# Performance work log

Measured on AMD Instinct MI355X. Metric: run time of the kernel, lower is better.

The kernel has to match this reference:

```python
import jax, jax.numpy as jnp
import numpy as np

N_NODES = 262144      # 2048 graphs * 128 nodes each
NUM_GRAPHS = 2048
MAX_NODES = 128
HIDDEN = 256
OUT_CH = 12
N_EDGES = 2097152     # ~avg degree 8


def setup_inputs() -> dict:
    key = jax.random.key(0)
    k1, k2, k3, k4 = jax.random.split(key, 4)
    x = jax.random.normal(k1, (N_NODES, HIDDEN), dtype=jnp.float32)
    # xavier-ish projection weight for Linear(6*hidden -> 12)
    W = jax.random.normal(k2, (OUT_CH, 6 * HIDDEN), dtype=jnp.float32) * (1.0 / np.sqrt(6 * HIDDEN))
    b = jnp.zeros((OUT_CH,), dtype=jnp.float32)
    # uniform graphs: sorted batch ids, MAX_NODES nodes per graph
    batch = (jnp.arange(N_NODES, dtype=jnp.int32) // MAX_NODES).astype(jnp.int32)
    # edges sampled within graphs: pick graph, then two local node ids
    g = jax.random.randint(k3, (N_EDGES,), 0, NUM_GRAPHS, dtype=jnp.int32)
    loc = jax.random.randint(k4, (N_EDGES, 2), 0, MAX_NODES, dtype=jnp.int32)
    src = g * MAX_NODES + loc[:, 0]
    dst = g * MAX_NODES + loc[:, 1]
    edge_index = jnp.stack([src, dst], axis=0).astype(jnp.int32)
    return {"x": x, "W": W, "b": b, "batch": batch, "edge_index": edge_index,
            "num_graphs": NUM_GRAPHS, "max_nodes": MAX_NODES}


def reference(x, W, b, batch, edge_index, num_graphs, max_nodes):
    N, H = x.shape
    G, M = num_graphs, max_nodes
    # local index of each node within its graph (batch is sorted by graph)
    counts = jax.ops.segment_sum(jnp.ones((N,), dtype=jnp.int32), batch, num_segments=G)
    starts = jnp.cumsum(counts) - counts            # exclusive prefix sum => first node of each graph
    local = jnp.arange(N, dtype=jnp.int32) - starts[batch]
    # dense per-graph node features X [G, M, H]
    X = jnp.zeros((G, M, H), dtype=x.dtype).at[batch, local].set(x)
    # dense symmetric adjacency A [G, M, M] (assignment semantics, like the torch loop)
    gi = batch[edge_index[0]]
    li = local[edge_index[0]]
    lj = local[edge_index[1]]
    A = jnp.zeros((G, M, M), dtype=x.dtype)
    A = A.at[gi, li, lj].set(1.0)
    A = A.at[gi, lj, li].set(1.0)
    # 6-gram walk readouts
    walk = X
    vs = [walk.sum(axis=1)]                          # v1
    for _ in range(5):                               # v2..v6
        walk = jnp.einsum('gnm,gmh->gnh', A, walk) * X
        vs.append(walk.sum(axis=1))
    out = jnp.concatenate(vs, axis=-1)               # == stack(dim=1).reshape(G, 6*H)
    out = out @ W.T + b                              # n_gram_projection
    return out
```

## Files before the change

### kernel.cpp

```cpp
#include <hip/hip_runtime.h>
#include <stdint.h>

#define NGRAPH 2048
#define MNODES 128
#define HID 256
#define OUTC 12
#define NEDGE 2097152

typedef __attribute__((ext_vector_type(8))) short short8;
typedef __attribute__((ext_vector_type(4))) float v4f;

#define SLICE 64
#define SWT_STRIDE 136

__device__ __forceinline__ unsigned short f2bf(float f) {
    unsigned int u = __builtin_bit_cast(unsigned int, f);
    u += 0x7fffu + ((u >> 16) & 1u);
    return (unsigned short)(u >> 16);
}

__global__ void build_bytes(const int* __restrict__ ei, unsigned char* __restrict__ Ab) {
    int e = blockIdx.x * blockDim.x + threadIdx.x;
    if (e >= NEDGE) return;
    int sN = ei[e];
    int dN = ei[NEDGE + e];
    int g = sN >> 7;
    int li = sN & 127;
    int lj = dN & 127;
    unsigned char* base = Ab + (size_t)g * (MNODES * MNODES);
    base[li * 128 + lj] = 1;
    base[lj * 128 + li] = 1;
}

__global__ void build_bits(const int* __restrict__ ei, unsigned int* __restrict__ bits) {
    int e = blockIdx.x * blockDim.x + threadIdx.x;
    if (e >= NEDGE) return;
    int sN = ei[e];
    int dN = ei[NEDGE + e];
    int g = sN >> 7;
    int li = sN & 127;
    int lj = dN & 127;
    unsigned int* base = bits + (size_t)g * (MNODES * 4);
    atomicOr(&base[li * 4 + (lj >> 5)], 1u << (lj & 31));
    atomicOr(&base[lj * 4 + (li >> 5)], 1u << (li & 31));
}

__launch_bounds__(256, 3)
__global__ void walk2(const float* __restrict__ x,
                      const float* __restrict__ W,
                      const unsigned char* __restrict__ Abytes,
                      const unsigned int* __restrict__ Abits,
                      int use_bytes,
                      float* __restrict__ partial) {
    __shared__ unsigned short sWT[SLICE][SWT_STRIDE];
    __shared__ float sVs2[2][6][SLICE];

    const int bx = blockIdx.x;
    const int g = bx >> 2;
    const int s = bx & 3;
    const int tid = threadIdx.x;
    const int wave = tid >> 6;
    const int lane = tid & 63;
    const int lrow = lane & 15;
    const int quad = lane >> 4;
    const int rhalf = wave >> 1;
    const int r0 = rhalf * 64;
    const int c0 = (wave & 1) * 32;
    const int cg0 = s * SLICE + c0;

    short8 areg[4][4];
    if (use_bytes) {
        const unsigned char* Ag = Abytes + (size_t)g * (MNODES * MNODES);
#pragma unroll
        for (int rt = 0; rt < 4; rt++) {
            int row = r0 + rt * 16 + lrow;
#pragma unroll
            for (int ks = 0; ks < 4; ks++) {
                int k0 = ks * 32 + quad * 8;
                uint2 u = *(const uint2*)(Ag + row * 128 + k0);
                short8 a;
#pragma unroll
                for (int j = 0; j < 8; j++) {
                    unsigned int byte = ((j < 4 ? u.x >> (8 * j) : u.y >> (8 * (j - 4))) & 0xFFu);
                    a[j] = (short)(byte ? 0x3F80 : 0);
                }
                areg[rt][ks] = a;
            }
        }
    } else {
        const unsigned int* Bg = Abits + (size_t)g * (MNODES * 4);
#pragma unroll
        for (int rt = 0; rt < 4; rt++) {
            int row = r0 + rt * 16 + lrow;
#pragma unroll
            for (int ks = 0; ks < 4; ks++) {
                unsigned int w = Bg[row * 4 + ks] >> (quad * 8);
                short8 a;
#pragma unroll
                for (int j = 0; j < 8; j++)
                    a[j] = (short)(((w >> j) & 1u) ? 0x3F80 : 0);
                areg[rt][ks] = a;
            }
        }
    }

    float xf[4][2][4];
    const float* xg = x + (size_t)g * (MNODES * HID);
#pragma unroll
    for (int rt = 0; rt < 4; rt++)
#pragma unroll
        for (int ct = 0; ct < 2; ct++) {
            int col = cg0 + ct * 16 + lrow;
#pragma unroll
            for (int reg = 0; reg < 4; reg++) {
                int row = r0 + rt * 16 + quad * 4 + reg;
                xf[rt][ct][reg] = xg[row * HID + col];
            }
        }
#pragma unroll
    for (int ct = 0; ct < 2; ct++) {
        int lcol = c0 + ct * 16 + lrow;
        float cs = 0.0f;
#pragma unroll
        for (int rt = 0; rt < 4; rt++) {
            int nbase = r0 + rt * 16 + quad * 4;
            uint2 u;
            u.x = (unsigned)f2bf(xf[rt][ct][0]) | ((unsigned)f2bf(xf[rt][ct][1]) << 16);
            u.y = (unsigned)f2bf(xf[rt][ct][2]) | ((unsigned)f2bf(xf[rt][ct][3]) << 16);
            *(uint2*)&sWT[lcol][nbase] = u;
            cs += xf[rt][ct][0] + xf[rt][ct][1] + xf[rt][ct][2] + xf[rt][ct][3];
        }
        cs += __shfl_xor(cs, 16);
        cs += __shfl_xor(cs, 32);
        if (quad == 0) sVs2[rhalf][0][lcol] = cs;
    }
    __syncthreads();

    for (int it = 1; it <= 5; it++) {
        v4f acc[4][2];
#pragma unroll
        for (int rt = 0; rt < 4; rt++)
#pragma unroll
            for (int ct = 0; ct < 2; ct++) acc[rt][ct] = (v4f)(0.0f);
#pragma unroll
        for (int ks = 0; ks < 4; ks++) {
            int k0 = ks * 32 + quad * 8;
#pragma unroll
            for (int ct = 0; ct < 2; ct++) {
                short8 bf = *(const short8*)&sWT[c0 + ct * 16 + lrow][k0];
#pragma unroll
                for (int rt = 0; rt < 4; rt++)
                    acc[rt][ct] = __builtin_amdgcn_mfma_f32_16x16x32_bf16(areg[rt][ks], bf, acc[rt][ct], 0, 0, 0);
            }
        }
        __syncthreads();
#pragma unroll
        for (int ct = 0; ct < 2; ct++) {
            int lcol = c0 + ct * 16 + lrow;
            float cs = 0.0f;
#pragma unroll
            for (int rt = 0; rt < 4; rt++) {
                float nw0 = acc[rt][ct][0] * xf[rt][ct][0];
                float nw1 = acc[rt][ct][1] * xf[rt][ct][1];
                float nw2 = acc[rt][ct][2] * xf[rt][ct][2];
                float nw3 = acc[rt][ct][3] * xf[rt][ct][3];
                int nbase = r0 + rt * 16 + quad * 4;
                uint2 u;
                u.x = (unsigned)f2bf(nw0) | ((unsigned)f2bf(nw1) << 16);
                u.y = (unsigned)f2bf(nw2) | ((unsigned)f2bf(nw3) << 16);
                *(uint2*)&sWT[lcol][nbase] = u;
                cs += nw0 + nw1 + nw2 + nw3;
            }
            cs += __shfl_xor(cs, 16);
            cs += __shfl_xor(cs, 32);
            if (quad == 0) sVs2[rhalf][it][lcol] = cs;
        }
        __syncthreads();
    }

    if (wave == 0) {
        for (int c = 0; c < OUTC; c++) {
            float p = 0.0f;
            const float* wr = W + c * (6 * HID);
#pragma unroll
            for (int ii = 0; ii < 6; ii++) {
                int i = ii * 64 + lane;
                int k = i >> 6;
                int h = i & 63;
                float v = sVs2[0][k][h] + sVs2[1][k][h];
                p += v * wr[k * HID + s * SLICE + h];
            }
#pragma unroll
            for (int off = 32; off >= 1; off >>= 1) p += __shfl_down(p, off);
            if (lane == 0) partial[bx * OUTC + c] = p;
        }
    }
}

__global__ void combine(const float* __restrict__ partial, const float* __restrict__ bvec,
                        float* __restrict__ out) {
    int i = blockIdx.x * blockDim.x + threadIdx.x;
    if (i >= NGRAPH * OUTC) return;
    int c = i % OUTC;
    int g = i / OUTC;
    float p = bvec[c];
#pragma unroll
    for (int s = 0; s < 4; s++) p += partial[(g * 4 + s) * OUTC + c];
    out[i] = p;
}

extern "C" void kernel_launch(void* const* d_in, const int* in_sizes, int n_in,
                              void* d_out, int out_size, void* d_ws, size_t ws_size,
                              hipStream_t stream) {
    const float* x = (const float*)d_in[0];
    const float* W = (const float*)d_in[1];
    const float* b = (const float*)d_in[2];
    const int* ei = (const int*)d_in[4];
    float* out = (float*)d_out;

    const size_t ABYTES = (size_t)NGRAPH * MNODES * MNODES;
    const size_t PARTIAL = (size_t)NGRAPH * 4 * OUTC * sizeof(float);

    if (ws_size >= ABYTES + PARTIAL) {
        unsigned char* Ab = (unsigned char*)d_ws;
        float* partial = (float*)((char*)d_ws + ABYTES);
        hipMemsetAsync(Ab, 0, ABYTES, stream);
        build_bytes<<<NEDGE / 256, 256, 0, stream>>>(ei, Ab);
        walk2<<<NGRAPH * 4, 256, 0, stream>>>(x, W, Ab, nullptr, 1, partial);
        combine<<<(NGRAPH * OUTC + 255) / 256, 256, 0, stream>>>(partial, b, out);
    } else {
        unsigned int* bits = (unsigned int*)d_ws;
        float* partial = (float*)((char*)d_ws + (size_t)NGRAPH * MNODES * 4 * 4);
        hipMemsetAsync(bits, 0, (size_t)NGRAPH * MNODES * 4 * 4, stream);
        build_bits<<<NEDGE / 512, 512, 0, stream>>>(ei, bits);
        walk2<<<NGRAPH * 4, 256, 0, stream>>>(x, W, nullptr, bits, 0, partial);
        combine<<<(NGRAPH * OUTC + 255) / 256, 256, 0, stream>>>(partial, b, out);
    }
}
```

Baseline: 502.6 us.

## Always use bitmask adjacency, hardware bf16 packing, and spread projection across waves

Drops the byte-per-entry adjacency path, which needs a 32MB memset and scatter plus 32MB of reads, and always builds a packed bitmask (4MB) with atomicOr. Each row's bitmask is now read as a single uint4. The manual round-to-nearest bf16 conversion is replaced with the v_cvt_pk_bf16_f32 instruction. The final projection is split across all four waves (three outputs each) instead of only wave 0, and launch bounds are raised to 5 blocks per SM, which risks register spills. Atomics in the bit build may contend within each graph's 2KB region.

```diff
diff --git a/kernel.cpp b/kernel.cpp
--- a/kernel.cpp
+++ b/kernel.cpp
@@ -13,23 +13,10 @@
 #define SLICE 64
 #define SWT_STRIDE 136
 
-__device__ __forceinline__ unsigned short f2bf(float f) {
-    unsigned int u = __builtin_bit_cast(unsigned int, f);
-    u += 0x7fffu + ((u >> 16) & 1u);
-    return (unsigned short)(u >> 16);
-}
-
-__global__ void build_bytes(const int* __restrict__ ei, unsigned char* __restrict__ Ab) {
-    int e = blockIdx.x * blockDim.x + threadIdx.x;
-    if (e >= NEDGE) return;
-    int sN = ei[e];
-    int dN = ei[NEDGE + e];
-    int g = sN >> 7;
-    int li = sN & 127;
-    int lj = dN & 127;
-    unsigned char* base = Ab + (size_t)g * (MNODES * MNODES);
-    base[li * 128 + lj] = 1;
-    base[lj * 128 + li] = 1;
+__device__ __forceinline__ unsigned int cvtpk_bf16(float lo, float hi) {
+    unsigned int r;
+    asm("v_cvt_pk_bf16_f32 %0, %1, %2" : "=v"(r) : "v"(lo), "v"(hi));
+    return r;
 }
 
 __global__ void build_bits(const int* __restrict__ ei, unsigned int* __restrict__ bits) {
@@ -45,12 +32,10 @@
     atomicOr(&base[lj * 4 + (li >> 5)], 1u << (li & 31));
 }
 
-__launch_bounds__(256, 3)
+__launch_bounds__(256, 5)
 __global__ void walk2(const float* __restrict__ x,
                       const float* __restrict__ W,
-                      const unsigned char* __restrict__ Abytes,
                       const unsigned int* __restrict__ Abits,
-                      int use_bytes,
                       float* __restrict__ partial) {
     __shared__ unsigned short sWT[SLICE][SWT_STRIDE];
     __shared__ float sVs2[2][6][SLICE];
@@ -69,32 +54,14 @@
     const int cg0 = s * SLICE + c0;
 
     short8 areg[4][4];
-    if (use_bytes) {
-        const unsigned char* Ag = Abytes + (size_t)g * (MNODES * MNODES);
+    {
+        const uint4* Bg = (const uint4*)(Abits + (size_t)g * (MNODES * 4));
 #pragma unroll
         for (int rt = 0; rt < 4; rt++) {
-            int row = r0 + rt * 16 + lrow;
+            uint4 w4 = Bg[r0 + rt * 16 + lrow];
 #pragma unroll
             for (int ks = 0; ks < 4; ks++) {
-                int k0 = ks * 32 + quad * 8;
-                uint2 u = *(const uint2*)(Ag + row * 128 + k0);
-                short8 a;
-#pragma unroll
-                for (int j = 0; j < 8; j++) {
-                    unsigned int byte = ((j < 4 ? u.x >> (8 * j) : u.y >> (8 * (j - 4))) & 0xFFu);
-                    a[j] = (short)(byte ? 0x3F80 : 0);
-                }
-                areg[rt][ks] = a;
-            }
-        }
-    } else {
-        const unsigned int* Bg = Abits + (size_t)g * (MNODES * 4);
-#pragma unroll
-        for (int rt = 0; rt < 4; rt++) {
-            int row = r0 + rt * 16 + lrow;
-#pragma unroll
-            for (int ks = 0; ks < 4; ks++) {
-                unsigned int w = Bg[row * 4 + ks] >> (quad * 8);
+                unsigned int w = (ks == 0 ? w4.x : ks == 1 ? w4.y : ks == 2 ? w4.z : w4.w) >> (quad * 8);
                 short8 a;
 #pragma unroll
                 for (int j = 0; j < 8; j++)
@@ -125,8 +92,8 @@
         for (int rt = 0; rt < 4; rt++) {
             int nbase = r0 + rt * 16 + quad * 4;
             uint2 u;
-            u.x = (unsigned)f2bf(xf[rt][ct][0]) | ((unsigned)f2bf(xf[rt][ct][1]) << 16);
-            u.y = (unsigned)f2bf(xf[rt][ct][2]) | ((unsigned)f2bf(xf[rt][ct][3]) << 16);
+            u.x = cvtpk_bf16(xf[rt][ct][0], xf[rt][ct][1]);
+            u.y = cvtpk_bf16(xf[rt][ct][2], xf[rt][ct][3]);
             *(uint2*)&sWT[lcol][nbase] = u;
             cs += xf[rt][ct][0] + xf[rt][ct][1] + xf[rt][ct][2] + xf[rt][ct][3];
         }
@@ -166,8 +133,8 @@
                 float nw3 = acc[rt][ct][3] * xf[rt][ct][3];
                 int nbase = r0 + rt * 16 + quad * 4;
                 uint2 u;
-                u.x = (unsigned)f2bf(nw0) | ((unsigned)f2bf(nw1) << 16);
-                u.y = (unsigned)f2bf(nw2) | ((unsigned)f2bf(nw3) << 16);
+                u.x = cvtpk_bf16(nw0, nw1);
+                u.y = cvtpk_bf16(nw2, nw3);
                 *(uint2*)&sWT[lcol][nbase] = u;
                 cs += nw0 + nw1 + nw2 + nw3;
             }
@@ -178,17 +145,17 @@
         __syncthreads();
     }
 
-    if (wave == 0) {
-        for (int c = 0; c < OUTC; c++) {
+    {
+        int cbase = wave * 3;
+#pragma unroll
+        for (int cc = 0; cc < 3; cc++) {
+            int c = cbase + cc;
+            const float* wr = W + c * (6 * HID) + s * SLICE;
             float p = 0.0f;
-            const float* wr = W + c * (6 * HID);
 #pragma unroll
-            for (int ii = 0; ii < 6; ii++) {
-                int i = ii * 64 + lane;
-                int k = i >> 6;
-                int h = i & 63;
-                float v = sVs2[0][k][h] + sVs2[1][k][h];
-                p += v * wr[k * HID + s * SLICE + h];
+            for (int k = 0; k < 6; k++) {
+                float v = sVs2[0][k][lane] + sVs2[1][k][lane];
+                p += v * wr[k * HID + lane];
             }
 #pragma unroll
             for (int off = 32; off >= 1; off >>= 1) p += __shfl_down(p, off);
@@ -218,22 +185,12 @@
     const int* ei = (const int*)d_in[4];
     float* out = (float*)d_out;
 
-    const size_t ABYTES = (size_t)NGRAPH * MNODES * MNODES;
-    const size_t PARTIAL = (size_t)NGRAPH * 4 * OUTC * sizeof(float);
+    const size_t BITS = (size_t)NGRAPH * MNODES * 4 * sizeof(unsigned int);
 
-    if (ws_size >= ABYTES + PARTIAL) {
-        unsigned char* Ab = (unsigned char*)d_ws;
-        float* partial = (float*)((char*)d_ws + ABYTES);
-        hipMemsetAsync(Ab, 0, ABYTES, stream);
-        build_bytes<<<NEDGE / 256, 256, 0, stream>>>(ei, Ab);
-        walk2<<<NGRAPH * 4, 256, 0, stream>>>(x, W, Ab, nullptr, 1, partial);
-        combine<<<(NGRAPH * OUTC + 255) / 256, 256, 0, stream>>>(partial, b, out);
-    } else {
-        unsigned int* bits = (unsigned int*)d_ws;
-        float* partial = (float*)((char*)d_ws + (size_t)NGRAPH * MNODES * 4 * 4);
-        hipMemsetAsync(bits, 0, (size_t)NGRAPH * MNODES * 4 * 4, stream);
-        build_bits<<<NEDGE / 512, 512, 0, stream>>>(ei, bits);
-        walk2<<<NGRAPH * 4, 256, 0, stream>>>(x, W, nullptr, bits, 0, partial);
-        combine<<<(NGRAPH * OUTC + 255) / 256, 256, 0, stream>>>(partial, b, out);
-    }
+    unsigned int* bits = (unsigned int*)d_ws;
+    float* partial = (float*)((char*)d_ws + BITS);
+    hipMemsetAsync(bits, 0, BITS, stream);
+    build_bits<<<NEDGE / 512, 512, 0, stream>>>(ei, bits);
+    walk2<<<NGRAPH * 4, 256, 0, stream>>>(x, W, bits, partial);
+    combine<<<(NGRAPH * OUTC + 255) / 256, 256, 0, stream>>>(partial, b, out);
 }
```

Result: slower. 900.4 us (+79.1%).
